# Optimization experiments

Measured on AMD Instinct MI355X. Metric: run time of the kernel, lower is better.

Reference implementation:

```python
import jax, jax.numpy as jnp
import numpy as np

N, DIN, DOUT = 8192, 4096, 4096

def setup_inputs() -> dict:
    key = jax.random.key(0)
    k1, k2 = jax.random.split(key)
    x = jax.random.normal(k1, (N, DIN), dtype=jnp.float32)
    # ternary-ish weights; forward applies sign() via STE anyway
    weight = jax.random.normal(k2, (DOUT, DIN), dtype=jnp.float32)
    bias = jnp.zeros((DOUT,), dtype=jnp.float32)
    scale = jnp.ones((1,), dtype=jnp.float32)  # scale_init = 1.0
    return {"x": x, "weight": weight, "bias": bias, "scale": scale}


def reference(x, weight, bias, scale):
    # STE sign-quantization: value is sign(weight) in {-1,0,1},
    # gradient flows to weight as identity.
    w = weight - jax.lax.stop_gradient(weight - jnp.sign(weight))
    # fused ternary matmul + scale + bias: out = scale * (x @ w.T + bias)
    # (backward in the torch code scales grad for x, w, AND bias, implying
    #  bias sits inside the scale multiplier)
    return scale[0] * (jnp.matmul(x, w.T) + bias)
```

## Files before the change

### kernel.cpp

```cpp
#include <hip/hip_runtime.h>
#include <hip/hip_bf16.h>
#include <stdint.h>

#define M_DIM 8192
#define K_DIM 4096
#define N_DIM 4096

typedef int intx4  __attribute__((ext_vector_type(4)));
typedef int intx16 __attribute__((ext_vector_type(16)));

__global__ void cvt_fused_i8_kernel(const float* __restrict__ x,
                                    const float* __restrict__ w,
                                    signed char* __restrict__ xb,
                                    signed char* __restrict__ wb,
                                    float* __restrict__ row_scale) {
    const int b   = blockIdx.x;
    const int tid = threadIdx.x;
    if (b < M_DIM) {
        __shared__ float wmax[4];
        const float* xr = x + (size_t)b * K_DIM;
        float4 v[4];
#pragma unroll
        for (int i = 0; i < 4; ++i)
            v[i] = *(const float4*)(xr + tid * 4 + i * 1024);

        float am = 0.f;
#pragma unroll
        for (int i = 0; i < 4; ++i) {
            am = fmaxf(am, fabsf(v[i].x)); am = fmaxf(am, fabsf(v[i].y));
            am = fmaxf(am, fabsf(v[i].z)); am = fmaxf(am, fabsf(v[i].w));
        }
#pragma unroll
        for (int off = 32; off > 0; off >>= 1)
            am = fmaxf(am, __shfl_xor(am, off));
        if ((tid & 63) == 0) wmax[tid >> 6] = am;
        __syncthreads();
        am = fmaxf(fmaxf(wmax[0], wmax[1]), fmaxf(wmax[2], wmax[3]));
        am = fmaxf(am, 1e-30f);

        const float inv = 127.f / am;
#pragma unroll
        for (int i = 0; i < 4; ++i) {
            union { signed char c[4]; uint32_t u; } r;
            const float* vf = (const float*)&v[i];
#pragma unroll
            for (int k = 0; k < 4; ++k) {
                int q = (int)rintf(vf[k] * inv);
                q = q > 127 ? 127 : (q < -127 ? -127 : q);
                r.c[k] = (signed char)q;
            }
            *(uint32_t*)(xb + (size_t)b * K_DIM + tid * 4 + i * 1024) = r.u;
        }
        if (tid == 0) row_scale[b] = am * (1.f / 127.f);
    } else {
        size_t t = ((size_t)(b - M_DIM) * blockDim.x + tid) * 8;
        float4 a = *(const float4*)(w + t);
        float4 c = *(const float4*)(w + t + 4);
        union { signed char s[8]; uint2 u; } r;
        r.s[0] = (a.x > 0.f) - (a.x < 0.f); r.s[1] = (a.y > 0.f) - (a.y < 0.f);
        r.s[2] = (a.z > 0.f) - (a.z < 0.f); r.s[3] = (a.w > 0.f) - (a.w < 0.f);
        r.s[4] = (c.x > 0.f) - (c.x < 0.f); r.s[5] = (c.y > 0.f) - (c.y < 0.f);
        r.s[6] = (c.z > 0.f) - (c.z < 0.f); r.s[7] = (c.w > 0.f) - (c.w < 0.f);
        *(uint2*)(wb + t) = r.u;
    }
}

__device__ __forceinline__ void gld_lds16(const void* g, void* l) {
    __builtin_amdgcn_global_load_lds(
        (const __attribute__((address_space(1))) void*)g,
        (__attribute__((address_space(3))) void*)l,
        16, 0, 0);
}

__global__ void __launch_bounds__(512, 2)
gemm_i8_kernel(const signed char* __restrict__ A,
               const signed char* __restrict__ B,
               const float* __restrict__ bias,
               const float* __restrict__ scale,
               const float* __restrict__ row_scale,
               float* __restrict__ out) {
    __shared__ __attribute__((aligned(16))) signed char sA[4][256 * 64];
    __shared__ __attribute__((aligned(16))) signed char sB[4][256 * 64];

    const int tid  = threadIdx.x;
    const int lane = tid & 63;
    const int wave = tid >> 6;
    const int wm = wave >> 2;
    const int wn = wave & 3;
    const int r5 = lane & 31;
    const int hi = lane >> 5;

    const int bid = blockIdx.x;
    const int swz = (bid & 7) * 64 + (bid >> 3);
    const int rowBase = (swz >> 4) * 256;
    const int colBase = (swz & 15) * 256;

    const int sc   = (lane & 3) ^ ((lane >> 3) & 3) ^ ((wave & 1) << 1);
    const int srow = wave * 16 + (lane >> 2);
    const signed char* gA0 = A + (size_t)(rowBase + srow) * K_DIM + sc * 16;
    const signed char* gA1 = gA0 + (size_t)128 * K_DIM;
    const signed char* gB0 = B + (size_t)(colBase + srow) * K_DIM + sc * 16;
    const signed char* gB1 = gB0 + (size_t)128 * K_DIM;
    const int ldsR0 = wave * 1024;
    const int ldsR1 = 8192 + wave * 1024;

    const int fsw = ((r5 >> 1) & 3) ^ (((r5 >> 4) & 1) << 1);
    const int ckE = ((hi + 0) ^ fsw) * 16;
    const int ckO = ((hi + 2) ^ fsw) * 16;
    const int aOff = (wm * 128 + r5) * 64;
    const int bOff = (wn * 64 + r5) * 64;

    intx16 acc[4][2] = {};

#pragma unroll
    for (int s = 0; s < 3; ++s) {
        const size_t kg = (size_t)s * 64;
        gld_lds16(gA0 + kg, &sA[s][ldsR0]);
        gld_lds16(gA1 + kg, &sA[s][ldsR1]);
        gld_lds16(gB0 + kg, &sB[s][ldsR0]);
        gld_lds16(gB1 + kg, &sB[s][ldsR1]);
    }
    asm volatile("s_waitcnt vmcnt(8)" ::: "memory");
    __builtin_amdgcn_s_barrier();

    for (int t = 0; t < 64; ++t) {
        const signed char* sAb = sA[t & 3];
        const signed char* sBb = sB[t & 3];
        signed char* pA = sA[(t + 3) & 3];
        signed char* pB = sB[(t + 3) & 3];
        const size_t kg = (size_t)(t + 3) * 64;
        const bool stage = t < 61;

        intx4 fa[4], fb[2];
#pragma unroll
        for (int mt = 0; mt < 4; ++mt)
            fa[mt] = *(const intx4*)(sAb + aOff + mt * 2048 + ckE);
#pragma unroll
        for (int nt = 0; nt < 2; ++nt)
            fb[nt] = *(const intx4*)(sBb + bOff + nt * 2048 + ckE);
        if (stage) {
            gld_lds16(gA0 + kg, pA + ldsR0);
            gld_lds16(gA1 + kg, pA + ldsR1);
        }
        __builtin_amdgcn_sched_barrier(0);
        __builtin_amdgcn_s_barrier();
        asm volatile("s_waitcnt lgkmcnt(0)" ::: "memory");
        __builtin_amdgcn_sched_barrier(0);
        __builtin_amdgcn_s_setprio(1);
#pragma unroll
        for (int mt = 0; mt < 4; ++mt)
#pragma unroll
            for (int nt = 0; nt < 2; ++nt)
                acc[mt][nt] = __builtin_amdgcn_mfma_i32_32x32x32_i8(
                    fa[mt], fb[nt], acc[mt][nt], 0, 0, 0);
        __builtin_amdgcn_s_setprio(0);
        __builtin_amdgcn_sched_barrier(0);
        __builtin_amdgcn_s_barrier();

        intx4 oa[4], ob[2];
#pragma unroll
        for (int mt = 0; mt < 4; ++mt)
            oa[mt] = *(const intx4*)(sAb + aOff + mt * 2048 + ckO);
#pragma unroll
        for (int nt = 0; nt < 2; ++nt)
            ob[nt] = *(const intx4*)(sBb + bOff + nt * 2048 + ckO);
        if (stage) {
            gld_lds16(gB0 + kg, pB + ldsR0);
            gld_lds16(gB1 + kg, pB + ldsR1);
        }
        __builtin_amdgcn_sched_barrier(0);
        __builtin_amdgcn_s_barrier();
        asm volatile("s_waitcnt lgkmcnt(0)" ::: "memory");
        __builtin_amdgcn_sched_barrier(0);
        __builtin_amdgcn_s_setprio(1);
#pragma unroll
        for (int mt = 0; mt < 4; ++mt)
#pragma unroll
            for (int nt = 0; nt < 2; ++nt)
                acc[mt][nt] = __builtin_amdgcn_mfma_i32_32x32x32_i8(
                    oa[mt], ob[nt], acc[mt][nt], 0, 0, 0);
        __builtin_amdgcn_s_setprio(0);
        __builtin_amdgcn_sched_barrier(0);

        if (t < 61)       asm volatile("s_waitcnt vmcnt(8)" ::: "memory");
        else if (t == 61) asm volatile("s_waitcnt vmcnt(4)" ::: "memory");
        else if (t == 62) asm volatile("s_waitcnt vmcnt(0)" ::: "memory");
        __builtin_amdgcn_s_barrier();
    }

    const float s = scale[0];
#pragma unroll
    for (int nt = 0; nt < 2; ++nt) {
        const int gcol = colBase + wn * 64 + nt * 32 + r5;
        const float bv = bias[gcol];
#pragma unroll
        for (int mt = 0; mt < 4; ++mt) {
#pragma unroll
            for (int q = 0; q < 4; ++q) {
                const int row0 = rowBase + wm * 128 + mt * 32 + q * 8 + hi * 4;
                const float4 rs4 = *(const float4*)(row_scale + row0);
                const float rs[4] = {rs4.x, rs4.y, rs4.z, rs4.w};
#pragma unroll
                for (int r = 0; r < 4; ++r)
                    __builtin_nontemporal_store(
                        s * ((float)acc[mt][nt][q * 4 + r] * rs[r] + bv),
                        out + (size_t)(row0 + r) * N_DIM + gcol);
            }
        }
    }
}

__global__ void fallback_kernel(const float* __restrict__ x,
                                const float* __restrict__ w,
                                const float* __restrict__ bias,
                                const float* __restrict__ scale,
                                float* __restrict__ out) {
    int col = blockIdx.x * 64 + (threadIdx.x & 63);
    int row = blockIdx.y * 4 + (threadIdx.x >> 6);
    const float* xr = x + (size_t)row * K_DIM;
    const float* wr = w + (size_t)col * K_DIM;
    float acc = 0.f;
    for (int k = 0; k < K_DIM; k += 4) {
        float4 a = *(const float4*)(xr + k);
        float4 b = *(const float4*)(wr + k);
        acc += a.x * (b.x > 0.f ? 1.f : (b.x < 0.f ? -1.f : 0.f));
        acc += a.y * (b.y > 0.f ? 1.f : (b.y < 0.f ? -1.f : 0.f));
        acc += a.z * (b.z > 0.f ? 1.f : (b.z < 0.f ? -1.f : 0.f));
        acc += a.w * (b.w > 0.f ? 1.f : (b.w < 0.f ? -1.f : 0.f));
    }
    out[(size_t)row * N_DIM + col] = scale[0] * (acc + bias[col]);
}

extern "C" void kernel_launch(void* const* d_in, const int* in_sizes, int n_in,
                              void* d_out, int out_size, void* d_ws, size_t ws_size,
                              hipStream_t stream) {
    const float* x     = (const float*)d_in[0];
    const float* w     = (const float*)d_in[1];
    const float* bias  = (const float*)d_in[2];
    const float* scale = (const float*)d_in[3];
    float* out = (float*)d_out;

    const size_t xb_bytes = (size_t)M_DIM * K_DIM;
    const size_t wb_bytes = (size_t)N_DIM * K_DIM;
    const size_t need = xb_bytes + wb_bytes + M_DIM * sizeof(float);

    if (ws_size >= need) {
        signed char* xb = (signed char*)d_ws;
        signed char* wb = xb + xb_bytes;
        float* row_scale = (float*)(wb + wb_bytes);
        const unsigned w_blocks = (unsigned)((size_t)N_DIM * K_DIM / 8 / 256);
        cvt_fused_i8_kernel<<<dim3(M_DIM + w_blocks), 256, 0, stream>>>(
            x, w, xb, wb, row_scale);
        gemm_i8_kernel<<<dim3((M_DIM / 256) * (N_DIM / 256)), 512, 0, stream>>>(
            xb, wb, bias, scale, row_scale, out);
    } else {
        dim3 grid(N_DIM / 64, M_DIM / 4);
        fallback_kernel<<<grid, 256, 0, stream>>>(x, w, bias, scale, out);
    }
}
```

Before: 403.2 us.

## Shrink GEMM tile to 256x128 with 3-stage pipeline and merged K-halves

```diff
diff --git a/kernel.cpp b/kernel.cpp
--- a/kernel.cpp
+++ b/kernel.cpp
@@ -72,109 +72,93 @@
         16, 0, 0);
 }
 
-__global__ void __launch_bounds__(512, 2)
+__global__ void __launch_bounds__(512, 4)
 gemm_i8_kernel(const signed char* __restrict__ A,
                const signed char* __restrict__ B,
                const float* __restrict__ bias,
                const float* __restrict__ scale,
                const float* __restrict__ row_scale,
                float* __restrict__ out) {
-    __shared__ __attribute__((aligned(16))) signed char sA[4][256 * 64];
-    __shared__ __attribute__((aligned(16))) signed char sB[4][256 * 64];
+    __shared__ __attribute__((aligned(16))) signed char sA[3][256 * 64];
+    __shared__ __attribute__((aligned(16))) signed char sB[3][128 * 64];
 
     const int tid  = threadIdx.x;
     const int lane = tid & 63;
     const int wave = tid >> 6;
-    const int wm = wave >> 2;
-    const int wn = wave & 3;
+    const int wm = wave >> 1;
+    const int wn = wave & 1;
     const int r5 = lane & 31;
     const int hi = lane >> 5;
 
     const int bid = blockIdx.x;
-    const int swz = (bid & 7) * 64 + (bid >> 3);
-    const int rowBase = (swz >> 4) * 256;
-    const int colBase = (swz & 15) * 256;
+    const int swz = (bid & 7) * 128 + (bid >> 3);
+    const int rowBase = (swz >> 5) * 256;
+    const int colBase = (swz & 31) * 128;
 
     const int sc   = (lane & 3) ^ ((lane >> 3) & 3) ^ ((wave & 1) << 1);
     const int srow = wave * 16 + (lane >> 2);
     const signed char* gA0 = A + (size_t)(rowBase + srow) * K_DIM + sc * 16;
     const signed char* gA1 = gA0 + (size_t)128 * K_DIM;
     const signed char* gB0 = B + (size_t)(colBase + srow) * K_DIM + sc * 16;
-    const signed char* gB1 = gB0 + (size_t)128 * K_DIM;
-    const int ldsR0 = wave * 1024;
-    const int ldsR1 = 8192 + wave * 1024;
+    const int ldsA0 = wave * 1024;
+    const int ldsA1 = 8192 + wave * 1024;
+    const int ldsB0 = wave * 1024;
 
     const int fsw = ((r5 >> 1) & 3) ^ (((r5 >> 4) & 1) << 1);
-    const int ckE = ((hi + 0) ^ fsw) * 16;
-    const int ckO = ((hi + 2) ^ fsw) * 16;
-    const int aOff = (wm * 128 + r5) * 64;
+    const int ck0 = ((hi + 0) ^ fsw) * 16;
+    const int ck1 = ((hi + 2) ^ fsw) * 16;
+    const int aOff = (wm * 64 + r5) * 64;
     const int bOff = (wn * 64 + r5) * 64;
 
-    intx16 acc[4][2] = {};
-
-#pragma unroll
-    for (int s = 0; s < 3; ++s) {
+    intx16 acc[2][2] = {};
+
+#pragma unroll
+    for (int s = 0; s < 2; ++s) {
         const size_t kg = (size_t)s * 64;
-        gld_lds16(gA0 + kg, &sA[s][ldsR0]);
-        gld_lds16(gA1 + kg, &sA[s][ldsR1]);
-        gld_lds16(gB0 + kg, &sB[s][ldsR0]);
-        gld_lds16(gB1 + kg, &sB[s][ldsR1]);
-    }
-    asm volatile("s_waitcnt vmcnt(8)" ::: "memory");
+        gld_lds16(gA0 + kg, &sA[s][ldsA0]);
+        gld_lds16(gA1 + kg, &sA[s][ldsA1]);
+        gld_lds16(gB0 + kg, &sB[s][ldsB0]);
+    }
+    asm volatile("s_waitcnt vmcnt(3)" ::: "memory");
     __builtin_amdgcn_s_barrier();
 
+    int sr = 0;
+    int sw = 2;
     for (int t = 0; t < 64; ++t) {
-        const signed char* sAb = sA[t & 3];
-        const signed char* sBb = sB[t & 3];
-        signed char* pA = sA[(t + 3) & 3];
-        signed char* pB = sB[(t + 3) & 3];
-        const size_t kg = (size_t)(t + 3) * 64;
-        const bool stage = t < 61;
-
-        intx4 fa[4], fb[2];
-#pragma unroll
-        for (int mt = 0; mt < 4; ++mt)
-            fa[mt] = *(const intx4*)(sAb + aOff + mt * 2048 + ckE);
-#pragma unroll
-        for (int nt = 0; nt < 2; ++nt)
-            fb[nt] = *(const intx4*)(sBb + bOff + nt * 2048 + ckE);
-        if (stage) {
-            gld_lds16(gA0 + kg, pA + ldsR0);
-            gld_lds16(gA1 + kg, pA + ldsR1);
+        const signed char* sAb = sA[sr];
+        const signed char* sBb = sB[sr];
+
+        intx4 fa[2], fb[2], oa[2], ob[2];
+#pragma unroll
+        for (int mt = 0; mt < 2; ++mt) {
+            fa[mt] = *(const intx4*)(sAb + aOff + mt * 2048 + ck0);
+            oa[mt] = *(const intx4*)(sAb + aOff + mt * 2048 + ck1);
+        }
+#pragma unroll
+        for (int nt = 0; nt < 2; ++nt) {
+            fb[nt] = *(const intx4*)(sBb + bOff + nt * 2048 + ck0);
+            ob[nt] = *(const intx4*)(sBb + bOff + nt * 2048 + ck1);
+        }
+        if (t <= 61) {
+            const size_t kg = (size_t)(t + 2) * 64;
+            gld_lds16(gA0 + kg, &sA[sw][ldsA0]);
+            gld_lds16(gA1 + kg, &sA[sw][ldsA1]);
+            gld_lds16(gB0 + kg, &sB[sw][ldsB0]);
         }
         __builtin_amdgcn_sched_barrier(0);
         __builtin_amdgcn_s_barrier();
         asm volatile("s_waitcnt lgkmcnt(0)" ::: "memory");
         __builtin_amdgcn_sched_barrier(0);
+
         __builtin_amdgcn_s_setprio(1);
 #pragma unroll
-        for (int mt = 0; mt < 4; ++mt)
+        for (int mt = 0; mt < 2; ++mt)
 #pragma unroll
             for (int nt = 0; nt < 2; ++nt)
                 acc[mt][nt] = __builtin_amdgcn_mfma_i32_32x32x32_i8(
                     fa[mt], fb[nt], acc[mt][nt], 0, 0, 0);
-        __builtin_amdgcn_s_setprio(0);
-        __builtin_amdgcn_sched_barrier(0);
-        __builtin_amdgcn_s_barrier();
-
-        intx4 oa[4], ob[2];
-#pragma unroll
-        for (int mt = 0; mt < 4; ++mt)
-            oa[mt] = *(const intx4*)(sAb + aOff + mt * 2048 + ckO);
-#pragma unroll
-        for (int nt = 0; nt < 2; ++nt)
-            ob[nt] = *(const intx4*)(sBb + bOff + nt * 2048 + ckO);
-        if (stage) {
-            gld_lds16(gB0 + kg, pB + ldsR0);
-            gld_lds16(gB1 + kg, pB + ldsR1);
-        }
-        __builtin_amdgcn_sched_barrier(0);
-        __builtin_amdgcn_s_barrier();
-        asm volatile("s_waitcnt lgkmcnt(0)" ::: "memory");
-        __builtin_amdgcn_sched_barrier(0);
-        __builtin_amdgcn_s_setprio(1);
-#pragma unroll
-        for (int mt = 0; mt < 4; ++mt)
+#pragma unroll
+        for (int mt = 0; mt < 2; ++mt)
 #pragma unroll
             for (int nt = 0; nt < 2; ++nt)
                 acc[mt][nt] = __builtin_amdgcn_mfma_i32_32x32x32_i8(
@@ -182,10 +166,12 @@
         __builtin_amdgcn_s_setprio(0);
         __builtin_amdgcn_sched_barrier(0);
 
-        if (t < 61)       asm volatile("s_waitcnt vmcnt(8)" ::: "memory");
-        else if (t == 61) asm volatile("s_waitcnt vmcnt(4)" ::: "memory");
+        if (t <= 61)      asm volatile("s_waitcnt vmcnt(3)" ::: "memory");
         else if (t == 62) asm volatile("s_waitcnt vmcnt(0)" ::: "memory");
         __builtin_amdgcn_s_barrier();
+
+        sr = (sr == 2) ? 0 : sr + 1;
+        sw = (sw == 2) ? 0 : sw + 1;
     }
 
     const float s = scale[0];
@@ -194,10 +180,10 @@
         const int gcol = colBase + wn * 64 + nt * 32 + r5;
         const float bv = bias[gcol];
 #pragma unroll
-        for (int mt = 0; mt < 4; ++mt) {
+        for (int mt = 0; mt < 2; ++mt) {
 #pragma unroll
             for (int q = 0; q < 4; ++q) {
-                const int row0 = rowBase + wm * 128 + mt * 32 + q * 8 + hi * 4;
+                const int row0 = rowBase + wm * 64 + mt * 32 + q * 8 + hi * 4;
                 const float4 rs4 = *(const float4*)(row_scale + row0);
                 const float rs[4] = {rs4.x, rs4.y, rs4.z, rs4.w};
 #pragma unroll
@@ -251,7 +237,7 @@
         const unsigned w_blocks = (unsigned)((size_t)N_DIM * K_DIM / 8 / 256);
         cvt_fused_i8_kernel<<<dim3(M_DIM + w_blocks), 256, 0, stream>>>(
             x, w, xb, wb, row_scale);
-        gemm_i8_kernel<<<dim3((M_DIM / 256) * (N_DIM / 256)), 512, 0, stream>>>(
+        gemm_i8_kernel<<<dim3((M_DIM / 256) * (N_DIM / 128)), 512, 0, stream>>>(
             xb, wb, bias, scale, row_scale, out);
     } else {
         dim3 grid(N_DIM / 64, M_DIM / 4);
```

Result: no change. 406.2 us (+0.7%).

## Restructure int8 GEMM pipeline to 3-stage ring with one barrier per iteration

Applied to the files above, without the earlier changes.

```diff
diff --git a/kernel.cpp b/kernel.cpp
--- a/kernel.cpp
+++ b/kernel.cpp
@@ -79,8 +79,8 @@
                const float* __restrict__ scale,
                const float* __restrict__ row_scale,
                float* __restrict__ out) {
-    __shared__ __attribute__((aligned(16))) signed char sA[4][256 * 64];
-    __shared__ __attribute__((aligned(16))) signed char sB[4][256 * 64];
+    __shared__ __attribute__((aligned(16))) signed char sA[3][256 * 64];
+    __shared__ __attribute__((aligned(16))) signed char sB[3][256 * 64];
 
     const int tid  = threadIdx.x;
     const int lane = tid & 63;
@@ -113,23 +113,21 @@
     intx16 acc[4][2] = {};
 
 #pragma unroll
-    for (int s = 0; s < 3; ++s) {
+    for (int s = 0; s < 2; ++s) {
         const size_t kg = (size_t)s * 64;
         gld_lds16(gA0 + kg, &sA[s][ldsR0]);
         gld_lds16(gA1 + kg, &sA[s][ldsR1]);
         gld_lds16(gB0 + kg, &sB[s][ldsR0]);
         gld_lds16(gB1 + kg, &sB[s][ldsR1]);
     }
-    asm volatile("s_waitcnt vmcnt(8)" ::: "memory");
+    asm volatile("s_waitcnt vmcnt(4)" ::: "memory");
     __builtin_amdgcn_s_barrier();
 
+    int sr = 0;
+    int sw = 2;
     for (int t = 0; t < 64; ++t) {
-        const signed char* sAb = sA[t & 3];
-        const signed char* sBb = sB[t & 3];
-        signed char* pA = sA[(t + 3) & 3];
-        signed char* pB = sB[(t + 3) & 3];
-        const size_t kg = (size_t)(t + 3) * 64;
-        const bool stage = t < 61;
+        const signed char* sAb = sA[sr];
+        const signed char* sBb = sB[sr];
 
         intx4 fa[4], fb[2];
 #pragma unroll
@@ -138,14 +136,24 @@
 #pragma unroll
         for (int nt = 0; nt < 2; ++nt)
             fb[nt] = *(const intx4*)(sBb + bOff + nt * 2048 + ckE);
-        if (stage) {
-            gld_lds16(gA0 + kg, pA + ldsR0);
-            gld_lds16(gA1 + kg, pA + ldsR1);
-        }
-        __builtin_amdgcn_sched_barrier(0);
-        __builtin_amdgcn_s_barrier();
-        asm volatile("s_waitcnt lgkmcnt(0)" ::: "memory");
-        __builtin_amdgcn_sched_barrier(0);
+        __builtin_amdgcn_sched_barrier(0);
+
+        intx4 oa[4], ob[2];
+#pragma unroll
+        for (int mt = 0; mt < 4; ++mt)
+            oa[mt] = *(const intx4*)(sAb + aOff + mt * 2048 + ckO);
+#pragma unroll
+        for (int nt = 0; nt < 2; ++nt)
+            ob[nt] = *(const intx4*)(sBb + bOff + nt * 2048 + ckO);
+        if (t <= 61) {
+            const size_t kg = (size_t)(t + 2) * 64;
+            gld_lds16(gA0 + kg, &sA[sw][ldsR0]);
+            gld_lds16(gA1 + kg, &sA[sw][ldsR1]);
+            gld_lds16(gB0 + kg, &sB[sw][ldsR0]);
+            gld_lds16(gB1 + kg, &sB[sw][ldsR1]);
+        }
+        __builtin_amdgcn_sched_barrier(0);
+
         __builtin_amdgcn_s_setprio(1);
 #pragma unroll
         for (int mt = 0; mt < 4; ++mt)
@@ -155,23 +163,7 @@
                     fa[mt], fb[nt], acc[mt][nt], 0, 0, 0);
         __builtin_amdgcn_s_setprio(0);
         __builtin_amdgcn_sched_barrier(0);
-        __builtin_amdgcn_s_barrier();
-
-        intx4 oa[4], ob[2];
-#pragma unroll
-        for (int mt = 0; mt < 4; ++mt)
-            oa[mt] = *(const intx4*)(sAb + aOff + mt * 2048 + ckO);
-#pragma unroll
-        for (int nt = 0; nt < 2; ++nt)
-            ob[nt] = *(const intx4*)(sBb + bOff + nt * 2048 + ckO);
-        if (stage) {
-            gld_lds16(gB0 + kg, pB + ldsR0);
-            gld_lds16(gB1 + kg, pB + ldsR1);
-        }
-        __builtin_amdgcn_sched_barrier(0);
-        __builtin_amdgcn_s_barrier();
-        asm volatile("s_waitcnt lgkmcnt(0)" ::: "memory");
-        __builtin_amdgcn_sched_barrier(0);
+
         __builtin_amdgcn_s_setprio(1);
 #pragma unroll
         for (int mt = 0; mt < 4; ++mt)
@@ -182,10 +174,12 @@
         __builtin_amdgcn_s_setprio(0);
         __builtin_amdgcn_sched_barrier(0);
 
-        if (t < 61)       asm volatile("s_waitcnt vmcnt(8)" ::: "memory");
-        else if (t == 61) asm volatile("s_waitcnt vmcnt(4)" ::: "memory");
+        if (t <= 61)      asm volatile("s_waitcnt vmcnt(4)" ::: "memory");
         else if (t == 62) asm volatile("s_waitcnt vmcnt(0)" ::: "memory");
         __builtin_amdgcn_s_barrier();
+
+        sr = (sr == 2) ? 0 : sr + 1;
+        sw = (sw == 2) ? 0 : sw + 1;
     }
 
     const float s = scale[0];
```

After: 395.9 us (median of 2 runs). Within noise of the previous version (-1.8%).
